# Kernel optimization log

Hardware: AMD Instinct MI355X
Metric: run time of the kernel (lower is better)

The kernel has to match this reference:

```python
import jax, jax.numpy as jnp
import numpy as np

N = 50000      # nodes
E = 800000     # edges
DIN = 128      # input_dim
H = 128        # hidden_dim
DOUT = 64      # output_dim
G = 256        # graphs in batch
HOPS = 2       # num_hops
EPS = 1e-5     # BatchNorm eps


def setup_inputs() -> dict:
    key = jax.random.key(0)
    ks = jax.random.split(key, 16)
    w = lambda k, shape: jax.random.normal(k, shape, jnp.float32) * 0.05
    return dict(
        x=jax.random.normal(ks[0], (N, DIN), jnp.float32),
        edge_index=jax.random.randint(ks[1], (2, E), 0, N),
        batch=jnp.sort(jax.random.randint(ks[2], (N,), 0, G)),
        # preprocess FFNN (weights stored [in, out]; math == torch x @ W.T + b)
        pre_w1=w(ks[3], (DIN, H)), pre_b1=jnp.zeros((H,), jnp.float32),
        pre_w2=w(ks[4], (H, H)),   pre_b2=jnp.zeros((H,), jnp.float32),
        # per-hop GCNConv weight/bias
        conv_w=w(ks[5], (HOPS, H, H)), conv_b=jnp.zeros((HOPS, H), jnp.float32),
        # per-hop FFNN
        ffnn_w1=w(ks[6], (HOPS, H, H)), ffnn_b1=jnp.zeros((HOPS, H), jnp.float32),
        ffnn_w2=w(ks[7], (HOPS, H, H)), ffnn_b2=jnp.zeros((HOPS, H), jnp.float32),
        # per-hop BatchNorm affine params
        bn_gamma=jnp.ones((HOPS, H), jnp.float32), bn_beta=jnp.zeros((HOPS, H), jnp.float32),
        # postprocess FFNN
        post_w1=w(ks[8], (H, H)),    post_b1=jnp.zeros((H,), jnp.float32),
        post_w2=w(ks[9], (H, DOUT)), post_b2=jnp.zeros((DOUT,), jnp.float32),
    )


def _ffnn(x, w1, b1, w2, b2):
    # Linear -> GELU(exact, erf-based like nn.GELU) -> Linear
    return jax.nn.gelu(x @ w1 + b1, approximate=False) @ w2 + b2


def reference(x, edge_index, batch,
              pre_w1, pre_b1, pre_w2, pre_b2,
              conv_w, conv_b, ffnn_w1, ffnn_b1, ffnn_w2, ffnn_b2,
              bn_gamma, bn_beta,
              post_w1, post_b1, post_w2, post_b2):
    n = x.shape[0]
    loops = jnp.arange(n)
    # GCNConv default: add self-loops, symmetric D^-1/2 A D^-1/2 normalization
    src = jnp.concatenate([edge_index[0], loops])
    dst = jnp.concatenate([edge_index[1], loops])
    deg = jax.ops.segment_sum(jnp.ones(src.shape[0], x.dtype), dst, num_segments=n)
    dis = jnp.where(deg > 0, jax.lax.rsqrt(deg), 0.0)
    norm = dis[src] * dis[dst]  # [E+N]

    x = _ffnn(x, pre_w1, pre_b1, pre_w2, pre_b2)  # preprocess
    for i in range(HOPS):
        # GCNConv: (x W) gathered at src, scaled, scatter-added at dst, + bias
        xw = x @ conv_w[i]
        agg = jax.ops.segment_sum(xw[src] * norm[:, None], dst, num_segments=n) + conv_b[i]
        x = agg + x  # residual
        # BatchNorm1d (training-mode batch statistics, biased variance)
        mean = x.mean(axis=0)
        var = x.var(axis=0)
        x = (x - mean) * jax.lax.rsqrt(var + EPS) * bn_gamma[i] + bn_beta[i]
        # dropout treated as identity (deterministic reference)
        x = _ffnn(x, ffnn_w1[i], ffnn_b1[i], ffnn_w2[i], ffnn_b2[i]) + x
    # global_mean_pool over graph ids
    sums = jax.ops.segment_sum(x, batch, num_segments=G)
    cnt = jax.ops.segment_sum(jnp.ones(n, x.dtype), batch, num_segments=G)
    pooled = sums / jnp.maximum(cnt, 1.0)[:, None]
    return _ffnn(pooled, post_w1, post_b1, post_w2, post_b2)
```

## Files before the change

### kernel.cpp

```cpp
#include <hip/hip_runtime.h>
#include <hip/hip_bf16.h>
#include <math.h>

#define NN 50000
#define EE 800000
#define GG 256
#define FILLB ((EE + 255) / 256)

typedef short bf16x8 __attribute__((ext_vector_type(8)));
typedef float f32x4 __attribute__((ext_vector_type(4)));
typedef unsigned int u32x4 __attribute__((ext_vector_type(4)));

__device__ __forceinline__ unsigned short f2bf(float x) {
    __hip_bfloat16 h = __float2bfloat16(x);
    union { __hip_bfloat16 h; unsigned short u; } c; c.h = h; return c.u;
}
__device__ __forceinline__ float bf2f(unsigned short u) {
    union { unsigned int v; float f; } t; t.v = ((unsigned int)u) << 16; return t.f;
}
__device__ __forceinline__ float gelu_f(float v) {
    return 0.5f * v * (1.0f + erff(v * 0.70710678118654752f));
}
__device__ __forceinline__ int swz(int row, int bytecol) {
    return row * 256 + (bytecol ^ ((row & 7) << 4));
}

__global__ void k_deg(const int* __restrict__ dst, int* __restrict__ degi, int E) {
    int i = blockIdx.x * blockDim.x + threadIdx.x;
    if (i < E) atomicAdd(&degi[dst[i]], 1);
}
__global__ void k_scan1(const int* __restrict__ degi, int* __restrict__ incl,
                        int* __restrict__ bsum, int N) {
    __shared__ int sm[1024];
    int t = threadIdx.x, i = blockIdx.x * 1024 + t;
    int v = (i < N) ? degi[i] : 0;
    sm[t] = v;
    __syncthreads();
    for (int off = 1; off < 1024; off <<= 1) {
        int add = (t >= off) ? sm[t - off] : 0;
        __syncthreads();
        sm[t] += add;
        __syncthreads();
    }
    if (i < N) incl[i] = sm[t];
    if (t == 1023) bsum[blockIdx.x] = sm[t];
}
__global__ void k_scan3(const int* __restrict__ incl, const int* __restrict__ degi,
                        const int* __restrict__ bsum, float* __restrict__ dis,
                        int* __restrict__ rowstart, int N, int E, int nsb) {
    __shared__ int sboff;
    int t = threadIdx.x;
    if (t < 64) {
        int nb = blockIdx.x >> 2;
        int v = (t < nb && t < nsb) ? bsum[t] : 0;
        #pragma unroll
        for (int o = 1; o < 64; o <<= 1) v += __shfl_xor(v, o, 64);
        if (t == 0) sboff = v;
    }
    __syncthreads();
    int i = blockIdx.x * 256 + t;
    if (i < N) {
        rowstart[i] = incl[i] - degi[i] + sboff;
        dis[i] = rsqrtf((float)(degi[i] + 1));
    }
    if (i == 0) rowstart[N] = E;
}
__global__ void k_fillprep(const int* __restrict__ src, const int* __restrict__ dst,
                           const int* __restrict__ rowstart, int* __restrict__ fillc,
                           int* __restrict__ col,
                           const float* __restrict__ w0, const float* __restrict__ w1,
                           const float* __restrict__ w2, const float* __restrict__ w3,
                           const float* __restrict__ w4, const float* __restrict__ w5,
                           const float* __restrict__ w6, const float* __restrict__ w7,
                           unsigned short* __restrict__ Wt, int E) {
    int blk = blockIdx.x;
    if (blk < FILLB) {
        int i = blk * 256 + threadIdx.x;
        if (i < E) {
            int s = src[i], d = dst[i];
            int pos = rowstart[d] + atomicAdd(&fillc[d], 1);
            col[pos] = s;
        }
    } else {
        int b = (blk - FILLB) >> 6;
        const float* W = b == 0 ? w0 : b == 1 ? w1 : b == 2 ? w2 : b == 3 ? w3
                       : b == 4 ? w4 : b == 5 ? w5 : b == 6 ? w6 : w7;
        int tid = ((blk - FILLB) & 63) * 256 + threadIdx.x;
        int n = tid >> 7, k = tid & 127;
        *(unsigned short*)((char*)(Wt + (size_t)b * 16384) + swz(n, k * 2)) = f2bf(W[k * 128 + n]);
    }
}

__global__ __launch_bounds__(512) void k_mm(
    const float* __restrict__ A32, const unsigned short* __restrict__ A16,
    const unsigned short* __restrict__ W1, const float* __restrict__ b1,
    const unsigned short* __restrict__ W2, const float* __restrict__ b2,
    const unsigned short* __restrict__ W3, const float* __restrict__ disv,
    const float* __restrict__ st_sum, const float* __restrict__ st_sq,
    const float* __restrict__ st_g, const float* __restrict__ st_b,
    float invN, int bn, int hasres,
    unsigned short* __restrict__ outxbf, unsigned short* __restrict__ out3,
    const int* __restrict__ batch, float* __restrict__ pooled, int M)
{
    __shared__ unsigned short As[128 * 128];
    __shared__ unsigned short Ws[128 * 128];
    __shared__ float lsc[128], lsh[128];
    __shared__ float sdis[128];
    __shared__ int gid[128];
    const int tid = threadIdx.x;
    const int bm = blockIdx.x * 128;
    if (st_sum && tid < 128) {
        float m = st_sum[tid] * invN;
        float var = st_sq[tid] * invN - m * m;
        float s = st_g[tid] * rsqrtf(var + 1e-5f);
        lsc[tid] = s;
        lsh[tid] = st_b[tid] - m * s;
    }
    __syncthreads();
    {
        const uint4* srcp = (const uint4*)W1;
        uint4* dstp = (uint4*)Ws;
        for (int i = tid; i < 2048; i += 512) dstp[i] = srcp[i];
    }
    #pragma unroll
    for (int pass = 0; pass < 4; ++pass) {
        int row = pass * 32 + (tid >> 4);
        int c8 = tid & 15;
        int gr = bm + row; if (gr > M - 1) gr = M - 1;
        float vv[8];
        if (A32) {
            const float* pp = A32 + (size_t)gr * 128 + c8 * 8;
            float4 v0 = *(const float4*)pp;
            float4 v1 = *(const float4*)(pp + 4);
            vv[0] = v0.x; vv[1] = v0.y; vv[2] = v0.z; vv[3] = v0.w;
            vv[4] = v1.x; vv[5] = v1.y; vv[6] = v1.z; vv[7] = v1.w;
        } else {
            u32x4 raw = __builtin_nontemporal_load((const u32x4*)(A16 + (size_t)gr * 128 + c8 * 8));
            #pragma unroll
            for (int d = 0; d < 4; ++d) {
                vv[2 * d]     = bf2f((unsigned short)(raw[d] & 0xffff));
                vv[2 * d + 1] = bf2f((unsigned short)(raw[d] >> 16));
            }
        }
        if (bn) {
            int ch = c8 * 8;
            #pragma unroll
            for (int j = 0; j < 8; ++j) vv[j] = vv[j] * lsc[ch + j] + lsh[ch + j];
        }
        unsigned short tmp[8];
        #pragma unroll
        for (int j = 0; j < 8; ++j) tmp[j] = f2bf(vv[j]);
        *(uint4*)((char*)As + swz(row, c8 * 16)) = *(uint4*)tmp;
    }
    __syncthreads();

    const int lane = tid & 63, wid = tid >> 6;
    const int r0 = wid * 16;
    const int lrow = lane & 15;
    const int lkb = (lane >> 4) * 16;
    const int cb = lane & 15;
    const int rb = r0 + (lane >> 4) * 4;

    f32x4 acc[8];
    #pragma unroll
    for (int n = 0; n < 8; ++n) acc[n] = (f32x4){0.f, 0.f, 0.f, 0.f};
    #pragma unroll
    for (int kk = 0; kk < 4; ++kk) {
        int bc = kk * 64 + lkb;
        bf16x8 a = *(const bf16x8*)((const char*)As + swz(r0 + lrow, bc));
        #pragma unroll
        for (int n = 0; n < 8; ++n) {
            bf16x8 b = *(const bf16x8*)((const char*)Ws + swz(n * 16 + lrow, bc));
            acc[n] = __builtin_amdgcn_mfma_f32_16x16x32_bf16(a, b, acc[n], 0, 0, 0);
        }
    }
    unsigned short rres[32];
    if (hasres) {
        #pragma unroll
        for (int n = 0; n < 8; ++n)
            #pragma unroll
            for (int j = 0; j < 4; ++j)
                rres[n * 4 + j] = *(const unsigned short*)((const char*)As + swz(rb + j, (n * 16 + cb) * 2));
    }
    #pragma unroll
    for (int n = 0; n < 8; ++n) {
        int colg = n * 16 + cb;
        float bv = b1[colg];
        #pragma unroll
        for (int j = 0; j < 4; ++j) {
            float v = gelu_f(acc[n][j] + bv);
            *(unsigned short*)((char*)As + swz(rb + j, colg * 2)) = f2bf(v);
        }
    }
    __syncthreads();
    {
        const uint4* srcp = (const uint4*)W2;
        uint4* dstp = (uint4*)Ws;
        for (int i = tid; i < 2048; i += 512) dstp[i] = srcp[i];
    }
    __syncthreads();
    #pragma unroll
    for (int n = 0; n < 8; ++n) acc[n] = (f32x4){0.f, 0.f, 0.f, 0.f};
    #pragma unroll
    for (int kk = 0; kk < 4; ++kk) {
        int bc = kk * 64 + lkb;
        bf16x8 a = *(const bf16x8*)((const char*)As + swz(r0 + lrow, bc));
        #pragma unroll
        for (int n = 0; n < 8; ++n) {
            bf16x8 b = *(const bf16x8*)((const char*)Ws + swz(n * 16 + lrow, bc));
            acc[n] = __builtin_amdgcn_mfma_f32_16x16x32_bf16(a, b, acc[n], 0, 0, 0);
        }
    }
    const int dopool = (pooled != nullptr);
    #pragma unroll
    for (int n = 0; n < 8; ++n) {
        int colg = n * 16 + cb;
        float bv = b2[colg];
        #pragma unroll
        for (int j = 0; j < 4; ++j) {
            int rowg = bm + rb + j;
            float v = acc[n][j] + bv;
            if (hasres) v += bf2f(rres[n * 4 + j]);
            acc[n][j] = v;
            if (outxbf && rowg < M) outxbf[(size_t)rowg * 128 + colg] = f2bf(v);
            if (W3) *(unsigned short*)((char*)As + swz(rb + j, colg * 2)) = f2bf(v);
        }
    }
    if (dopool) {
        __syncthreads();
        float* wsfA = (float*)As;
        float* wsfB = (float*)Ws;
        #pragma unroll
        for (int n = 0; n < 8; ++n)
            #pragma unroll
            for (int j = 0; j < 4; ++j) {
                int row = rb + j;
                float* dstrow = (row < 64) ? (wsfA + row * 128) : (wsfB + (row - 64) * 128);
                dstrow[n * 16 + cb] = acc[n][j];
            }
        if (tid < 128) { int r = bm + tid; gid[tid] = (r < M) ? batch[r] : -1; }
        __syncthreads();
        if (tid < 128) {
            float pacc = 0.f;
            int gcur = gid[0];
            for (int r = 0; r < 128; ++r) {
                int gg = gid[r];
                if (gg != gcur) {
                    if (gcur >= 0) atomicAdd(&pooled[(size_t)gcur * 128 + tid], pacc);
                    pacc = 0.f; gcur = gg;
                }
                if (gg >= 0) pacc += (r < 64) ? wsfA[r * 128 + tid] : wsfB[(r - 64) * 128 + tid];
            }
            if (gcur >= 0) atomicAdd(&pooled[(size_t)gcur * 128 + tid], pacc);
        }
        return;
    }
    if (!W3) return;
    __syncthreads();
    {
        const uint4* srcp = (const uint4*)W3;
        uint4* dstp = (uint4*)Ws;
        for (int i = tid; i < 2048; i += 512) dstp[i] = srcp[i];
        if (tid < 128) { int r = bm + tid; sdis[tid] = disv[(r < M) ? r : (M - 1)]; }
    }
    __syncthreads();
    #pragma unroll
    for (int n = 0; n < 8; ++n) acc[n] = (f32x4){0.f, 0.f, 0.f, 0.f};
    #pragma unroll
    for (int kk = 0; kk < 4; ++kk) {
        int bc = kk * 64 + lkb;
        bf16x8 a = *(const bf16x8*)((const char*)As + swz(r0 + lrow, bc));
        #pragma unroll
        for (int n = 0; n < 8; ++n) {
            bf16x8 b = *(const bf16x8*)((const char*)Ws + swz(n * 16 + lrow, bc));
            acc[n] = __builtin_amdgcn_mfma_f32_16x16x32_bf16(a, b, acc[n], 0, 0, 0);
        }
    }
    #pragma unroll
    for (int n = 0; n < 8; ++n) {
        int colg = n * 16 + cb;
        #pragma unroll
        for (int j = 0; j < 4; ++j) {
            int rowg = bm + rb + j;
            if (rowg < M) out3[(size_t)rowg * 128 + colg] = f2bf(acc[n][j] * sdis[rb + j]);
        }
    }
}

__global__ __launch_bounds__(256) void k_agg(
    const unsigned short* __restrict__ xws, const int* __restrict__ rowstart,
    const int* __restrict__ col,
    const float* __restrict__ dis, const float* __restrict__ convb,
    const unsigned short* __restrict__ x0, unsigned short* __restrict__ zbf,
    float* __restrict__ bnsum, float* __restrict__ bnsq, int N)
{
    __shared__ float redS[4][128];
    __shared__ float redQ[4][128];
    const int tid = threadIdx.x;
    const int lane = tid & 63;
    const int wid = tid >> 6;
    const int half = lane >> 5;
    const int hl = lane & 31;
    const int g2 = hl >> 4;
    const int cl = lane & 15;
    const int ch = cl * 8;
    const int wave = blockIdx.x * 4 + wid;
    const int nwaves = gridDim.x * 4;

    float cb[8];
    #pragma unroll
    for (int j = 0; j < 8; ++j) cb[j] = convb[ch + j];
    float s[8], q[8];
    #pragma unroll
    for (int j = 0; j < 8; ++j) { s[j] = 0.f; q[j] = 0.f; }

    for (int vb = wave * 2; vb < N; vb += nwaves * 2) {
        const int v = vb + half;
        const bool vvalid = v < N;
        int e0 = 0, e1 = 0;
        if (vvalid) { e0 = rowstart[v]; e1 = rowstart[v + 1]; }
        float dv = 0.f;
        u32x4 pself = (u32x4){0, 0, 0, 0};
        u32x4 x16 = (u32x4){0, 0, 0, 0};
        if (vvalid && g2 == 0) {
            dv = dis[v];
            pself = *(const u32x4*)(xws + (size_t)v * 128 + ch);
            x16 = __builtin_nontemporal_load((const u32x4*)(x0 + (size_t)v * 128 + ch));
        }
        float a[8];
        #pragma unroll
        for (int j = 0; j < 8; ++j) a[j] = 0.f;
        int e = e0 + g2;
        for (; e + 6 < e1; e += 8) {
            const int u0 = col[e];
            const int u1 = col[e + 2];
            const int u2 = col[e + 4];
            const int u3 = col[e + 6];
            u32x4 p0 = *(const u32x4*)(xws + (size_t)u0 * 128 + ch);
            u32x4 p1 = *(const u32x4*)(xws + (size_t)u1 * 128 + ch);
            u32x4 p2 = *(const u32x4*)(xws + (size_t)u2 * 128 + ch);
            u32x4 p3 = *(const u32x4*)(xws + (size_t)u3 * 128 + ch);
            #pragma unroll
            for (int d = 0; d < 4; ++d) {
                a[2 * d]     += bf2f((unsigned short)(p0[d] & 0xffff)) + bf2f((unsigned short)(p1[d] & 0xffff))
                              + bf2f((unsigned short)(p2[d] & 0xffff)) + bf2f((unsigned short)(p3[d] & 0xffff));
                a[2 * d + 1] += bf2f((unsigned short)(p0[d] >> 16)) + bf2f((unsigned short)(p1[d] >> 16))
                              + bf2f((unsigned short)(p2[d] >> 16)) + bf2f((unsigned short)(p3[d] >> 16));
            }
        }
        for (; e + 2 < e1; e += 4) {
            const int u0 = col[e];
            const int u1 = col[e + 2];
            u32x4 p0 = *(const u32x4*)(xws + (size_t)u0 * 128 + ch);
            u32x4 p1 = *(const u32x4*)(xws + (size_t)u1 * 128 + ch);
            #pragma unroll
            for (int d = 0; d < 4; ++d) {
                a[2 * d]     += bf2f((unsigned short)(p0[d] & 0xffff)) + bf2f((unsigned short)(p1[d] & 0xffff));
                a[2 * d + 1] += bf2f((unsigned short)(p0[d] >> 16)) + bf2f((unsigned short)(p1[d] >> 16));
            }
        }
        if (e < e1) {
            const int u = col[e];
            u32x4 p = *(const u32x4*)(xws + (size_t)u * 128 + ch);
            #pragma unroll
            for (int d = 0; d < 4; ++d) {
                a[2 * d]     += bf2f((unsigned short)(p[d] & 0xffff));
                a[2 * d + 1] += bf2f((unsigned short)(p[d] >> 16));
            }
        }
        #pragma unroll
        for (int j = 0; j < 8; ++j) a[j] += __shfl_xor(a[j], 16, 64);
        if (vvalid && g2 == 0) {
            float zz[8];
            #pragma unroll
            for (int d = 0; d < 4; ++d) {
                zz[2 * d]     = dv * (a[2 * d]     + bf2f((unsigned short)(pself[d] & 0xffff)));
                zz[2 * d + 1] = dv * (a[2 * d + 1] + bf2f((unsigned short)(pself[d] >> 16)));
            }
            const float xr[8] = {
                bf2f((unsigned short)(x16[0] & 0xffff)), bf2f((unsigned short)(x16[0] >> 16)),
                bf2f((unsigned short)(x16[1] & 0xffff)), bf2f((unsigned short)(x16[1] >> 16)),
                bf2f((unsigned short)(x16[2] & 0xffff)), bf2f((unsigned short)(x16[2] >> 16)),
                bf2f((unsigned short)(x16[3] & 0xffff)), bf2f((unsigned short)(x16[3] >> 16))
            };
            unsigned short zo[8];
            #pragma unroll
            for (int j = 0; j < 8; ++j) {
                zz[j] += cb[j] + xr[j];
                s[j] += zz[j];
                q[j] += zz[j] * zz[j];
                zo[j] = f2bf(zz[j]);
            }
            __builtin_nontemporal_store(*(const u32x4*)zo, (u32x4*)(zbf + (size_t)v * 128 + ch));
        }
    }
    #pragma unroll
    for (int j = 0; j < 8; ++j) {
        s[j] += __shfl_xor(s[j], 32, 64);
        q[j] += __shfl_xor(q[j], 32, 64);
    }
    if ((lane >> 4) == 0) {
        #pragma unroll
        for (int j = 0; j < 8; ++j) { redS[wid][ch + j] = s[j]; redQ[wid][ch + j] = q[j]; }
    }
    __syncthreads();
    if (tid < 128) {
        float ts = redS[0][tid] + redS[1][tid] + redS[2][tid] + redS[3][tid];
        float tq = redQ[0][tid] + redQ[1][tid] + redQ[2][tid] + redQ[3][tid];
        atomicAdd(&bnsum[tid], ts);
        atomicAdd(&bnsq[tid], tq);
    }
}
__global__ __launch_bounds__(128) void k_post(
    const float* __restrict__ pooled, const int* __restrict__ batch,
    const float* __restrict__ w1, const float* __restrict__ b1,
    const float* __restrict__ w2, const float* __restrict__ b2,
    float* __restrict__ out, int N, int G)
{
    __shared__ float pr[128], hr[128];
    __shared__ int bounds[2];
    int g = blockIdx.x, t = threadIdx.x;
    if (t < 2) {
        int tgt = g + t, lo = 0, hi = N;
        while (lo < hi) { int mid = (lo + hi) >> 1; if (batch[mid] < tgt) lo = mid + 1; else hi = mid; }
        bounds[t] = lo;
    }
    __syncthreads();
    float c = fmaxf((float)(bounds[1] - bounds[0]), 1.0f);
    pr[t] = pooled[(size_t)g * 128 + t] / c;
    __syncthreads();
    float a = b1[t];
    for (int k = 0; k < 128; ++k) a += pr[k] * w1[k * 128 + t];
    hr[t] = gelu_f(a);
    __syncthreads();
    if (t < 64) {
        float o = b2[t];
        for (int k = 0; k < 128; ++k) o += hr[k] * w2[k * 64 + t];
        out[g * 64 + t] = o;
    }
}

extern "C" void kernel_launch(void* const* d_in, const int* in_sizes, int n_in,
                              void* d_out, int out_size, void* d_ws, size_t ws_size,
                              hipStream_t stream) {
    (void)in_sizes; (void)n_in; (void)out_size; (void)ws_size;
    const float* x_in    = (const float*)d_in[0];
    const int*   ei      = (const int*)d_in[1];
    const int*   batch   = (const int*)d_in[2];
    const float* pre_w1  = (const float*)d_in[3];
    const float* pre_b1  = (const float*)d_in[4];
    const float* pre_w2  = (const float*)d_in[5];
    const float* pre_b2  = (const float*)d_in[6];
    const float* conv_w  = (const float*)d_in[7];
    const float* conv_b  = (const float*)d_in[8];
    const float* ffnn_w1 = (const float*)d_in[9];
    const float* ffnn_b1 = (const float*)d_in[10];
    const float* ffnn_w2 = (const float*)d_in[11];
    const float* ffnn_b2 = (const float*)d_in[12];
    const float* bn_gamma= (const float*)d_in[13];
    const float* bn_beta = (const float*)d_in[14];
    const float* post_w1 = (const float*)d_in[15];
    const float* post_b1 = (const float*)d_in[16];
    const float* post_w2 = (const float*)d_in[17];
    const float* post_b2 = (const float*)d_in[18];
    const int* srcE = ei;
    const int* dstE = ei + EE;

    char* base = (char*)d_ws;
    size_t off = 0;
    auto carve = [&](size_t bytes) {
        char* q = base + off;
        off = (off + bytes + 255) & ~(size_t)255;
        return q;
    };
    unsigned short* xbf = (unsigned short*)carve((size_t)NN * 128 * 2);
    unsigned short* zbf = (unsigned short*)carve((size_t)NN * 128 * 2);
    unsigned short* hbf = (unsigned short*)carve((size_t)NN * 128 * 2);
    float* dis   = (float*)carve((size_t)NN * 4);
    int*   degi  = (int*)carve((size_t)NN * 4);
    int*   fillc = (int*)carve((size_t)NN * 4);
    float* pooled= (float*)carve((size_t)GG * 128 * 4);
    float* bnstat= (float*)carve(512 * 4);
    size_t zlen  = (size_t)((char*)(bnstat + 512) - (char*)degi);
    int* incl    = (int*)carve((size_t)NN * 4);
    int* bsum    = (int*)carve(64 * 4);
    int* rowstart= (int*)carve((size_t)(NN + 1) * 4);
    int* colx    = (int*)carve((size_t)EE * 4);
    unsigned short* Wt = (unsigned short*)carve((size_t)8 * 16384 * 2);

    hipMemsetAsync(degi, 0, zlen, stream);

    const int nsb = (NN + 1023) / 1024;
    k_deg<<<(EE + 255) / 256, 256, 0, stream>>>(dstE, degi, EE);
    k_scan1<<<nsb, 1024, 0, stream>>>(degi, incl, bsum, NN);
    k_scan3<<<(NN + 255) / 256, 256, 0, stream>>>(incl, degi, bsum, dis, rowstart, NN, EE, nsb);
    k_fillprep<<<FILLB + 512, 256, 0, stream>>>(srcE, dstE, rowstart, fillc, colx,
                                                pre_w1, pre_w2, conv_w, conv_w + 16384,
                                                ffnn_w1, ffnn_w1 + 16384, ffnn_w2, ffnn_w2 + 16384,
                                                Wt, EE);

    const int gB = (NN + 127) / 128;
    const float invN = 1.0f / NN;
    k_mm<<<gB, 512, 0, stream>>>(x_in, nullptr, Wt + 0 * 16384, pre_b1, Wt + 1 * 16384, pre_b2,
                                 Wt + 2 * 16384, dis, nullptr, nullptr, nullptr, nullptr,
                                 invN, 0, 0, xbf, hbf, nullptr, nullptr, NN);
    k_agg<<<2048, 256, 0, stream>>>(hbf, rowstart, colx, dis, conv_b,
                                    xbf, zbf, bnstat, bnstat + 128, NN);
    k_mm<<<gB, 512, 0, stream>>>(nullptr, zbf, Wt + 4 * 16384, ffnn_b1, Wt + 6 * 16384, ffnn_b2,
                                 Wt + 3 * 16384, dis, bnstat, bnstat + 128, bn_gamma, bn_beta,
                                 invN, 1, 1, xbf, hbf, nullptr, nullptr, NN);
    k_agg<<<2048, 256, 0, stream>>>(hbf, rowstart, colx, dis, conv_b + 128,
                                    xbf, zbf, bnstat + 256, bnstat + 384, NN);
    k_mm<<<gB, 512, 0, stream>>>(nullptr, zbf, Wt + 5 * 16384, ffnn_b1 + 128, Wt + 7 * 16384, ffnn_b2 + 128,
                                 nullptr, nullptr, bnstat + 256, bnstat + 384, bn_gamma + 128, bn_beta + 128,
                                 invN, 1, 1, nullptr, nullptr, batch, pooled, NN);
    k_post<<<GG, 128, 0, stream>>>(pooled, batch, post_w1, post_b1, post_w2, post_b2,
                                   (float*)d_out, NN, GG);
}
```

Baseline: 340.0 us.

## Quantize GCN message features to int8 with per-row scales for gather

The X·W output feeding the sparse aggregation is now stored as int8 with a per-row float scale that folds in the degree normalization, replacing bf16. The aggregation kernel regroups lanes (8 lanes × 16 channels, 4 edge groups) and dequantizes gathered rows on the fly. The aim is to halve the bytes moved by the memory-bound random gather over 800k edges. In exchange it adds a row-max reduction and an LDS staging pass in the matmul epilogue, plus an extra scale load per edge, and it loses precision, which could exceed tolerance.

Result: slower. 360.4 us (+6.0%).

```diff
diff --git a/kernel.cpp b/kernel.cpp
--- a/kernel.cpp
+++ b/kernel.cpp
@@ -23,6 +23,16 @@
 }
 __device__ __forceinline__ int swz(int row, int bytecol) {
     return row * 256 + (bytecol ^ ((row & 7) << 4));
+}
+__device__ __forceinline__ void dq16(u32x4 p, float sc, float* a) {
+    #pragma unroll
+    for (int w = 0; w < 4; ++w) {
+        unsigned int x = p[w];
+        a[w * 4 + 0] += sc * (float)(int)(signed char)(x & 0xff);
+        a[w * 4 + 1] += sc * (float)(int)(signed char)((x >> 8) & 0xff);
+        a[w * 4 + 2] += sc * (float)(int)(signed char)((x >> 16) & 0xff);
+        a[w * 4 + 3] += sc * (float)(int)(signed char)(x >> 24);
+    }
 }
 
 __global__ void k_deg(const int* __restrict__ dst, int* __restrict__ degi, int E) {
@@ -99,7 +109,8 @@
     const float* __restrict__ st_sum, const float* __restrict__ st_sq,
     const float* __restrict__ st_g, const float* __restrict__ st_b,
     float invN, int bn, int hasres,
-    unsigned short* __restrict__ outxbf, unsigned short* __restrict__ out3,
+    unsigned short* __restrict__ outxbf,
+    char* __restrict__ out3q, float* __restrict__ outscale,
     const int* __restrict__ batch, float* __restrict__ pooled, int M)
 {
     __shared__ unsigned short As[128 * 128];
@@ -276,20 +287,41 @@
             acc[n] = __builtin_amdgcn_mfma_f32_16x16x32_bf16(a, b, acc[n], 0, 0, 0);
         }
     }
-    #pragma unroll
-    for (int n = 0; n < 8; ++n) {
-        int colg = n * 16 + cb;
-        #pragma unroll
-        for (int j = 0; j < 4; ++j) {
+    __syncthreads();
+    char* q8 = (char*)Ws;
+    #pragma unroll
+    for (int j = 0; j < 4; ++j) {
+        float rmax = 0.f;
+        #pragma unroll
+        for (int n = 0; n < 8; ++n) rmax = fmaxf(rmax, fabsf(acc[n][j]));
+        #pragma unroll
+        for (int o = 1; o < 16; o <<= 1) rmax = fmaxf(rmax, __shfl_xor(rmax, o, 64));
+        float inv = (rmax > 0.f) ? (127.0f / rmax) : 0.f;
+        #pragma unroll
+        for (int n = 0; n < 8; ++n) {
+            int qv = __float2int_rn(acc[n][j] * inv);
+            q8[(rb + j) * 128 + n * 16 + cb] = (char)qv;
+        }
+        if (cb == 0) {
             int rowg = bm + rb + j;
-            if (rowg < M) out3[(size_t)rowg * 128 + colg] = f2bf(acc[n][j] * sdis[rb + j]);
+            if (rowg < M) outscale[rowg] = rmax * (1.0f / 127.0f) * sdis[rb + j];
+        }
+    }
+    __syncthreads();
+    {
+        const u32x4* s4 = (const u32x4*)q8;
+        for (int i = tid; i < 1024; i += 512) {
+            int row = i >> 3;
+            int rowg = bm + row;
+            if (rowg < M)
+                *(u32x4*)(out3q + (size_t)rowg * 128 + (size_t)((i & 7) * 16)) = s4[i];
         }
     }
 }
 
 __global__ __launch_bounds__(256) void k_agg(
-    const unsigned short* __restrict__ xws, const int* __restrict__ rowstart,
-    const int* __restrict__ col,
+    const char* __restrict__ xq, const float* __restrict__ xscale,
+    const int* __restrict__ rowstart, const int* __restrict__ col,
     const float* __restrict__ dis, const float* __restrict__ convb,
     const unsigned short* __restrict__ x0, unsigned short* __restrict__ zbf,
     float* __restrict__ bnsum, float* __restrict__ bnsq, int N)
@@ -301,107 +333,97 @@
     const int wid = tid >> 6;
     const int half = lane >> 5;
     const int hl = lane & 31;
-    const int g2 = hl >> 4;
-    const int cl = lane & 15;
-    const int ch = cl * 8;
+    const int g4 = hl >> 3;
+    const int li = lane & 7;
+    const int ch = li * 16;
     const int wave = blockIdx.x * 4 + wid;
     const int nwaves = gridDim.x * 4;
 
-    float cb[8];
-    #pragma unroll
-    for (int j = 0; j < 8; ++j) cb[j] = convb[ch + j];
-    float s[8], q[8];
-    #pragma unroll
-    for (int j = 0; j < 8; ++j) { s[j] = 0.f; q[j] = 0.f; }
+    float cbv[16];
+    #pragma unroll
+    for (int k = 0; k < 16; ++k) cbv[k] = convb[ch + k];
+    float s[16], q[16];
+    #pragma unroll
+    for (int k = 0; k < 16; ++k) { s[k] = 0.f; q[k] = 0.f; }
 
     for (int vb = wave * 2; vb < N; vb += nwaves * 2) {
         const int v = vb + half;
         const bool vvalid = v < N;
         int e0 = 0, e1 = 0;
         if (vvalid) { e0 = rowstart[v]; e1 = rowstart[v + 1]; }
-        float dv = 0.f;
-        u32x4 pself = (u32x4){0, 0, 0, 0};
-        u32x4 x16 = (u32x4){0, 0, 0, 0};
-        if (vvalid && g2 == 0) {
+        float dv = 0.f, sself = 0.f;
+        u32x4 pselfq = (u32x4){0, 0, 0, 0};
+        u32x4 xa = (u32x4){0, 0, 0, 0}, xb = (u32x4){0, 0, 0, 0};
+        if (vvalid && hl < 8) {
             dv = dis[v];
-            pself = *(const u32x4*)(xws + (size_t)v * 128 + ch);
-            x16 = __builtin_nontemporal_load((const u32x4*)(x0 + (size_t)v * 128 + ch));
-        }
-        float a[8];
-        #pragma unroll
-        for (int j = 0; j < 8; ++j) a[j] = 0.f;
-        int e = e0 + g2;
-        for (; e + 6 < e1; e += 8) {
+            sself = xscale[v];
+            pselfq = *(const u32x4*)(xq + (size_t)v * 128 + ch);
+            xa = __builtin_nontemporal_load((const u32x4*)(x0 + (size_t)v * 128 + ch));
+            xb = __builtin_nontemporal_load((const u32x4*)(x0 + (size_t)v * 128 + ch + 8));
+        }
+        float a[16];
+        #pragma unroll
+        for (int k = 0; k < 16; ++k) a[k] = 0.f;
+        int e = e0 + g4;
+        for (; e + 12 < e1; e += 16) {
             const int u0 = col[e];
-            const int u1 = col[e + 2];
-            const int u2 = col[e + 4];
-            const int u3 = col[e + 6];
-            u32x4 p0 = *(const u32x4*)(xws + (size_t)u0 * 128 + ch);
-            u32x4 p1 = *(const u32x4*)(xws + (size_t)u1 * 128 + ch);
-            u32x4 p2 = *(const u32x4*)(xws + (size_t)u2 * 128 + ch);
-            u32x4 p3 = *(const u32x4*)(xws + (size_t)u3 * 128 + ch);
+            const int u1 = col[e + 4];
+            const int u2 = col[e + 8];
+            const int u3 = col[e + 12];
+            const float s0 = xscale[u0];
+            const float s1 = xscale[u1];
+            const float s2 = xscale[u2];
+            const float s3 = xscale[u3];
+            u32x4 p0 = *(const u32x4*)(xq + (size_t)u0 * 128 + ch);
+            u32x4 p1 = *(const u32x4*)(xq + (size_t)u1 * 128 + ch);
+            u32x4 p2 = *(const u32x4*)(xq + (size_t)u2 * 128 + ch);
+            u32x4 p3 = *(const u32x4*)(xq + (size_t)u3 * 128 + ch);
+            dq16(p0, s0, a);
+            dq16(p1, s1, a);
+            dq16(p2, s2, a);
+            dq16(p3, s3, a);
+        }
+        for (; e < e1; e += 4) {
+            const int u = col[e];
+            const float sc = xscale[u];
+            u32x4 p = *(const u32x4*)(xq + (size_t)u * 128 + ch);
+            dq16(p, sc, a);
+        }
+        #pragma unroll
+        for (int k = 0; k < 16; ++k) {
+            a[k] += __shfl_xor(a[k], 8, 64);
+            a[k] += __shfl_xor(a[k], 16, 64);
+        }
+        if (vvalid && hl < 8) {
+            dq16(pselfq, sself, a);
+            float xr[16];
             #pragma unroll
-            for (int d = 0; d < 4; ++d) {
-                a[2 * d]     += bf2f((unsigned short)(p0[d] & 0xffff)) + bf2f((unsigned short)(p1[d] & 0xffff))
-                              + bf2f((unsigned short)(p2[d] & 0xffff)) + bf2f((unsigned short)(p3[d] & 0xffff));
-                a[2 * d + 1] += bf2f((unsigned short)(p0[d] >> 16)) + bf2f((unsigned short)(p1[d] >> 16))
-                              + bf2f((unsigned short)(p2[d] >> 16)) + bf2f((unsigned short)(p3[d] >> 16));
+            for (int w = 0; w < 4; ++w) {
+                xr[2 * w]     = bf2f((unsigned short)(xa[w] & 0xffff));
+                xr[2 * w + 1] = bf2f((unsigned short)(xa[w] >> 16));
+                xr[8 + 2 * w]     = bf2f((unsigned short)(xb[w] & 0xffff));
+                xr[8 + 2 * w + 1] = bf2f((unsigned short)(xb[w] >> 16));
             }
-        }
-        for (; e + 2 < e1; e += 4) {
-            const int u0 = col[e];
-            const int u1 = col[e + 2];
-            u32x4 p0 = *(const u32x4*)(xws + (size_t)u0 * 128 + ch);
-            u32x4 p1 = *(const u32x4*)(xws + (size_t)u1 * 128 + ch);
+            unsigned short zo[16];
             #pragma unroll
-            for (int d = 0; d < 4; ++d) {
-                a[2 * d]     += bf2f((unsigned short)(p0[d] & 0xffff)) + bf2f((unsigned short)(p1[d] & 0xffff));
-                a[2 * d + 1] += bf2f((unsigned short)(p0[d] >> 16)) + bf2f((unsigned short)(p1[d] >> 16));
-            }
-        }
-        if (e < e1) {
-            const int u = col[e];
-            u32x4 p = *(const u32x4*)(xws + (size_t)u * 128 + ch);
-            #pragma unroll
-            for (int d = 0; d < 4; ++d) {
-                a[2 * d]     += bf2f((unsigned short)(p[d] & 0xffff));
-                a[2 * d + 1] += bf2f((unsigned short)(p[d] >> 16));
-            }
-        }
-        #pragma unroll
-        for (int j = 0; j < 8; ++j) a[j] += __shfl_xor(a[j], 16, 64);
-        if (vvalid && g2 == 0) {
-            float zz[8];
-            #pragma unroll
-            for (int d = 0; d < 4; ++d) {
-                zz[2 * d]     = dv * (a[2 * d]     + bf2f((unsigned short)(pself[d] & 0xffff)));
-                zz[2 * d + 1] = dv * (a[2 * d + 1] + bf2f((unsigned short)(pself[d] >> 16)));
-            }
-            const float xr[8] = {
-                bf2f((unsigned short)(x16[0] & 0xffff)), bf2f((unsigned short)(x16[0] >> 16)),
-                bf2f((unsigned short)(x16[1] & 0xffff)), bf2f((unsigned short)(x16[1] >> 16)),
-                bf2f((unsigned short)(x16[2] & 0xffff)), bf2f((unsigned short)(x16[2] >> 16)),
-                bf2f((unsigned short)(x16[3] & 0xffff)), bf2f((unsigned short)(x16[3] >> 16))
-            };
-            unsigned short zo[8];
-            #pragma unroll
-            for (int j = 0; j < 8; ++j) {
-                zz[j] += cb[j] + xr[j];
-                s[j] += zz[j];
-                q[j] += zz[j] * zz[j];
-                zo[j] = f2bf(zz[j]);
+            for (int k = 0; k < 16; ++k) {
+                float zz = dv * a[k] + cbv[k] + xr[k];
+                s[k] += zz;
+                q[k] += zz * zz;
+                zo[k] = f2bf(zz);
             }
             __builtin_nontemporal_store(*(const u32x4*)zo, (u32x4*)(zbf + (size_t)v * 128 + ch));
-        }
-    }
-    #pragma unroll
-    for (int j = 0; j < 8; ++j) {
-        s[j] += __shfl_xor(s[j], 32, 64);
-        q[j] += __shfl_xor(q[j], 32, 64);
-    }
-    if ((lane >> 4) == 0) {
-        #pragma unroll
-        for (int j = 0; j < 8; ++j) { redS[wid][ch + j] = s[j]; redQ[wid][ch + j] = q[j]; }
+            __builtin_nontemporal_store(*(const u32x4*)(zo + 8), (u32x4*)(zbf + (size_t)v * 128 + ch + 8));
+        }
+    }
+    #pragma unroll
+    for (int k = 0; k < 16; ++k) {
+        s[k] += __shfl_xor(s[k], 32, 64);
+        q[k] += __shfl_xor(q[k], 32, 64);
+    }
+    if (lane < 8) {
+        #pragma unroll
+        for (int k = 0; k < 16; ++k) { redS[wid][ch + k] = s[k]; redQ[wid][ch + k] = q[k]; }
     }
     __syncthreads();
     if (tid < 128) {
@@ -475,7 +497,8 @@
     };
     unsigned short* xbf = (unsigned short*)carve((size_t)NN * 128 * 2);
     unsigned short* zbf = (unsigned short*)carve((size_t)NN * 128 * 2);
-    unsigned short* hbf = (unsigned short*)carve((size_t)NN * 128 * 2);
+    char*  xq    = (char*)carve((size_t)NN * 128);
+    float* xscale= (float*)carve((size_t)NN * 4);
     float* dis   = (float*)carve((size_t)NN * 4);
     int*   degi  = (int*)carve((size_t)NN * 4);
     int*   fillc = (int*)carve((size_t)NN * 4);
@@ -503,17 +526,17 @@
     const float invN = 1.0f / NN;
     k_mm<<<gB, 512, 0, stream>>>(x_in, nullptr, Wt + 0 * 16384, pre_b1, Wt + 1 * 16384, pre_b2,
                                  Wt + 2 * 16384, dis, nullptr, nullptr, nullptr, nullptr,
-                                 invN, 0, 0, xbf, hbf, nullptr, nullptr, NN);
-    k_agg<<<2048, 256, 0, stream>>>(hbf, rowstart, colx, dis, conv_b,
+                                 invN, 0, 0, xbf, xq, xscale, nullptr, nullptr, NN);
+    k_agg<<<2048, 256, 0, stream>>>(xq, xscale, rowstart, colx, dis, conv_b,
                                     xbf, zbf, bnstat, bnstat + 128, NN);
     k_mm<<<gB, 512, 0, stream>>>(nullptr, zbf, Wt + 4 * 16384, ffnn_b1, Wt + 6 * 16384, ffnn_b2,
                                  Wt + 3 * 16384, dis, bnstat, bnstat + 128, bn_gamma, bn_beta,
-                                 invN, 1, 1, xbf, hbf, nullptr, nullptr, NN);
-    k_agg<<<2048, 256, 0, stream>>>(hbf, rowstart, colx, dis, conv_b + 128,
+                                 invN, 1, 1, xbf, xq, xscale, nullptr, nullptr, NN);
+    k_agg<<<2048, 256, 0, stream>>>(xq, xscale, rowstart, colx, dis, conv_b + 128,
                                     xbf, zbf, bnstat + 256, bnstat + 384, NN);
     k_mm<<<gB, 512, 0, stream>>>(nullptr, zbf, Wt + 5 * 16384, ffnn_b1 + 128, Wt + 7 * 16384, ffnn_b2 + 128,
                                  nullptr, nullptr, bnstat + 256, bnstat + 384, bn_gamma + 128, bn_beta + 128,
-                                 invN, 1, 1, nullptr, nullptr, batch, pooled, NN);
+                                 invN, 1, 1, nullptr, nullptr, nullptr, batch, pooled, NN);
     k_post<<<GG, 128, 0, stream>>>(pooled, batch, post_w1, post_b1, post_w2, post_b2,
                                    (float*)d_out, NN, GG);
 }
```
